# Kernel tuning notes

Hardware: AMD Instinct MI355X
Metric: run time of the kernel (lower is better)

## Reference

```python
import jax, jax.numpy as jnp
import numpy as np

D_MODEL = 2048
N_HEADS = 32
N_KVHEADS = 8
HEAD_DIM = D_MODEL // N_HEADS  # 64
N_GROUPS = N_HEADS // N_KVHEADS  # 4
B, L = 2, 2048


def setup_inputs() -> dict:
    key = jax.random.key(0)
    k1, k2, k3 = jax.random.split(key, 3)
    x = jax.random.normal(k1, (B, L, D_MODEL), dtype=jnp.float32)
    W_qkv = jax.random.normal(k2, (D_MODEL, HEAD_DIM * (N_HEADS + 2 * N_KVHEADS)), dtype=jnp.float32) * 0.02
    W_out = jax.random.normal(k3, (D_MODEL, D_MODEL), dtype=jnp.float32) * 0.02
    # additive causal mask, broadcasts over (b, g, h, l, j)
    neg = jnp.float32(-1e9)
    mask = jnp.where(jnp.tril(jnp.ones((L, L), dtype=bool)), jnp.float32(0.0), neg)
    return {"x": x, "mask": mask, "W_qkv": W_qkv, "W_out": W_out}


def reference(x, mask, W_qkv, W_out):
    b, l, _ = x.shape
    qkv = x @ W_qkv  # (b, l, hd*(H + 2*KVH))
    q, k, v = jnp.split(qkv, [N_HEADS * HEAD_DIM, (N_HEADS + N_KVHEADS) * HEAD_DIM], axis=-1)
    # NOTE: faithful to the original: plain row-major reshapes (no seq/head transpose)
    q = q.reshape(b, N_GROUPS, N_KVHEADS, l, HEAD_DIM)  # (b, g, h, l, d)
    k = k.reshape(b, N_KVHEADS, l, HEAD_DIM)            # (b, h, j, d)
    v = v.reshape(b, N_KVHEADS, l, HEAD_DIM)            # (b, h, j, d)
    scores = jnp.einsum('bghld,bhjd->bghlj', q, k) * (HEAD_DIM ** -0.5)
    scores = scores + mask  # mask broadcasts over leading dims
    attn = jax.nn.softmax(scores, axis=-1)
    out = jnp.einsum('bghlj,bhjd->bghld', attn, v)  # (b, g, h, l, d)
    # rearrange 'b g h l d -> b l (g h d)'
    out = jnp.transpose(out, (0, 3, 1, 2, 4)).reshape(b, l, D_MODEL)
    return out @ W_out
```

## Files before the change

kernel.cpp:

```cpp
#include <hip/hip_runtime.h>
#include <stdint.h>


typedef unsigned short u16;
typedef unsigned int u32;
typedef __attribute__((ext_vector_type(8))) short bf16x8;
typedef __attribute__((ext_vector_type(4))) float f32x4;

__device__ __forceinline__ u16 f2bf(float f) {
  union { float f; uint32_t u; } v; v.f = f;
  uint32_t u = v.u;
  u += 0x7fffu + ((u >> 16) & 1u);
  return (u16)(u >> 16);
}

__device__ __forceinline__ f32x4 mfma16(bf16x8 a, bf16x8 b, f32x4 c) {
  return __builtin_amdgcn_mfma_f32_16x16x32_bf16(a, b, c, 0, 0, 0);
}

__device__ __forceinline__ uint32_t cvt_pk_bf16(float a, float b) {
  uint32_t r;
  asm("v_cvt_pk_bf16_f32 %0, %1, %2" : "=v"(r) : "v"(a), "v"(b));
  return r;
}

__device__ __forceinline__ float fmax3(float a, float b, float c) {
  float d;
  asm("v_max3_f32 %0, %1, %2, %3" : "=v"(d) : "v"(a), "v"(b), "v"(c));
  return d;
}

__device__ __forceinline__ float exp2fast(float x) {
  return __builtin_amdgcn_exp2f(x);
}

__device__ __forceinline__ void gload16(const u16* g, u16* l) {
  __builtin_amdgcn_global_load_lds((__attribute__((address_space(1))) void*)g,
                                   (__attribute__((address_space(3))) void*)l, 16, 0, 0);
}

__global__ __launch_bounds__(256) void cvt_f32_bf16(const float* __restrict__ in,
                                                    u16* __restrict__ out, int n4) {
  int i = blockIdx.x * blockDim.x + threadIdx.x;
  if (i < n4) {
    float4 v = ((const float4*)in)[i];
    uint2 o;
    o.x = (uint32_t)f2bf(v.x) | ((uint32_t)f2bf(v.y) << 16);
    o.y = (uint32_t)f2bf(v.z) | ((uint32_t)f2bf(v.w) << 16);
    ((uint2*)out)[i] = o;
  }
}

__global__ __launch_bounds__(256) void transpose_cvt(const float* __restrict__ in,
                                                     u16* __restrict__ out, int R, int C) {
  __shared__ float tile[32][33];
  int c0 = blockIdx.x * 32, r0 = blockIdx.y * 32;
  int tx = threadIdx.x, ty = threadIdx.y;
#pragma unroll
  for (int k = 0; k < 32; k += 8)
    tile[ty + k][tx] = in[(size_t)(r0 + ty + k) * C + c0 + tx];
  __syncthreads();
#pragma unroll
  for (int k = 0; k < 32; k += 8)
    out[(size_t)(c0 + ty + k) * R + r0 + tx] = f2bf(tile[tx][ty + k]);
}

template <bool OUTF32>
__global__ __launch_bounds__(256) void gemm_bf16(const u16* __restrict__ A,
                                                 const u16* __restrict__ Bt,
                                                 void* __restrict__ C,
                                                 int M, int N, int K) {
  __shared__ __align__(16) u16 As[2][128 * 32];
  __shared__ __align__(16) u16 Bs[2][128 * 32];
  int tid = threadIdx.x;
  int lane = tid & 63, w = tid >> 6;
  int wm = (w >> 1) * 64, wn = (w & 1) * 64;

  int nwg = gridDim.x * gridDim.y;
  int lin = blockIdx.y * gridDim.x + blockIdx.x;
  int lin2 = (lin & 7) * (nwg >> 3) + (lin >> 3);
  int bxs = lin2 % gridDim.x, bys = lin2 / gridDim.x;
  int bm = bys * 128, bn = bxs * 128;

  int c = lane & 15, g = lane >> 4;

  const int srow = w * 16 + (lane >> 2);
  const int scol = (((lane & 3) ^ ((lane >> 3) & 3))) * 8;
  const u16* aP = A + (size_t)(bm + srow) * K + scol;
  const u16* bP = Bt + (size_t)(bn + srow) * K + scol;
  const size_t rowskip = (size_t)64 * K;

  f32x4 zero = {0.f, 0.f, 0.f, 0.f};
  f32x4 acc[4][4];
#pragma unroll
  for (int mi = 0; mi < 4; mi++)
#pragma unroll
    for (int ni = 0; ni < 4; ni++) acc[mi][ni] = zero;

  auto STAGE = [&](int kt, int buf) {
    u16* aL = &As[buf][(w * 16) * 32];
    u16* bL = &Bs[buf][(w * 16) * 32];
    gload16(aP + kt, aL);
    gload16(aP + kt + rowskip, aL + 64 * 32);
    gload16(bP + kt, bL);
    gload16(bP + kt + rowskip, bL + 64 * 32);
  };

  const int nk = K >> 5;
  STAGE(0, 0);
  __syncthreads();

  const int fq = (g ^ ((c >> 1) & 3)) * 8;

  for (int t = 0; t < nk; ++t) {
    const int cur = t & 1;
    if (t + 1 < nk) STAGE((t + 1) << 5, cur ^ 1);
    bf16x8 af[4], bfr[4];
#pragma unroll
    for (int i = 0; i < 4; i++) af[i] = *(const bf16x8*)&As[cur][(wm + i * 16 + c) * 32 + fq];
#pragma unroll
    for (int i = 0; i < 4; i++) bfr[i] = *(const bf16x8*)&Bs[cur][(wn + i * 16 + c) * 32 + fq];
#pragma unroll
    for (int mi = 0; mi < 4; mi++)
#pragma unroll
      for (int ni = 0; ni < 4; ni++)
        acc[mi][ni] = mfma16(af[mi], bfr[ni], acc[mi][ni]);
    __syncthreads();
  }

#pragma unroll
  for (int mi = 0; mi < 4; mi++)
#pragma unroll
    for (int ni = 0; ni < 4; ni++)
#pragma unroll
      for (int i = 0; i < 4; i++) {
        int row = bm + wm + mi * 16 + g * 4 + i;
        int col = bn + wn + ni * 16 + c;
        float v = acc[mi][ni][i];
        if (OUTF32)
          ((float*)C)[(size_t)row * N + col] = v;
        else
          ((u16*)C)[(size_t)row * N + col] = f2bf(v);
      }
}

__global__ __launch_bounds__(512, 4) void attn_fwd(const u16* __restrict__ qkv,
                                                   u16* __restrict__ attn) {
  __shared__ __align__(16) u16 Ks[2][64][72];
  __shared__ __align__(16) u16 Vs[2][64][72];
  __shared__ __align__(16) u16 Ps[8][2][16][64];
  const int tid = threadIdx.x;
  const int lane = tid & 63, w = tid >> 6;
  const int c = lane & 15, g = lane >> 4;
  const float C2 = 0.18033688011112042f;

  const int bid = blockIdx.x;
  const int slot = bid >> 3;
  const int head = (bid & 7) * 8 + (slot >> 3);
  const int p = slot & 7;
  const int qtA = p, qtB = 15 - p;
  const int b = head >> 5, gh = head & 31, h = gh & 7;
  const u16* qb = qkv + (size_t)b * 6291456;
  const int qbaseA = qtA * 128 + w * 16;
  const int qbaseB = qtB * 128 + w * 16;

  const u16* qpA = qb + (size_t)(gh * 64 + qtA * 4 + (w >> 1)) * 3072 + ((w & 1) * 16 + c) * 64;
  const u16* qpB = qb + (size_t)(gh * 64 + qtB * 4 + (w >> 1)) * 3072 + ((w & 1) * 16 + c) * 64;
  bf16x8 qfA[2], qfB[2];
#pragma unroll
  for (int kd = 0; kd < 2; kd++) {
    qfA[kd] = *(const bf16x8*)(qpA + kd * 32 + g * 8);
    qfB[kd] = *(const bf16x8*)(qpB + kd * 32 + g * 8);
  }

  const f32x4 zero = {0.f, 0.f, 0.f, 0.f};
  f32x4 oA[4], oB[4];
#pragma unroll
  for (int dt = 0; dt < 4; dt++) { oA[dt] = zero; oB[dt] = zero; }
  float mA = -1e30f, sA = 0.f, mB = -1e30f, sB = 0.f;

  const int kj = tid >> 3, kd8 = (tid & 7) * 8;
  const int ksw = (kj & 7) << 3;
  const int vj0 = (tid & 31) * 2, vd = (tid >> 5) * 4;
  uint4 kreg;
  uint2 va, vb;

  auto LOAD = [&](int t) {
    int j = t * 64 + kj;
    const u16* kr = qb + (size_t)(h * 256 + (j >> 3)) * 3072 + 2048 + (j & 7) * 64;
    kreg = *(const uint4*)(kr + kd8);
    int jv0 = t * 64 + vj0;
    const u16* vr0 = qb + (size_t)(h * 256 + (jv0 >> 3)) * 3072 + 2560 + (jv0 & 7) * 64;
    int jv1 = jv0 + 1;
    const u16* vr1 = qb + (size_t)(h * 256 + (jv1 >> 3)) * 3072 + 2560 + (jv1 & 7) * 64;
    va = *(const uint2*)(vr0 + vd);
    vb = *(const uint2*)(vr1 + vd);
  };
  auto EX = [](uint2 v, int e) -> uint32_t {
    uint32_t x = (e < 2) ? v.x : v.y;
    return (e & 1) ? (x >> 16) : (x & 0xffffu);
  };
  auto STORE = [&](int buf) {
    *(uint4*)&Ks[buf][kj][kd8 ^ ksw] = kreg;
#pragma unroll
    for (int e = 0; e < 4; e++) {
      uint32_t wv = EX(va, e) | (EX(vb, e) << 16);
      int d = vd + e;
      *(u32*)&Vs[buf][d][vj0 ^ ((d & 7) << 3)] = wv;
    }
  };

  auto scorePart = [&](int t, int qbase, bf16x8 (&qf)[2], bf16x8 (&kf)[4][2],
                       float& m_i, float& s_i, f32x4 (&o)[4], int part) {
    f32x4 sc[4];
    __builtin_amdgcn_s_setprio(1);
#pragma unroll
    for (int kvt = 0; kvt < 4; kvt++) {
      f32x4 s = mfma16(kf[kvt][0], qf[0], zero);
      sc[kvt] = mfma16(kf[kvt][1], qf[1], s);
    }
    __builtin_amdgcn_s_setprio(0);
    const int q = qbase + c;
    if (t * 64 + 63 > qbase) {
#pragma unroll
      for (int kvt = 0; kvt < 4; kvt++)
#pragma unroll
        for (int i = 0; i < 4; i++)
          if (t * 64 + kvt * 16 + g * 4 + i > q) sc[kvt][i] = -1e30f;
    }
    float tmax = fmax3(sc[0][0], sc[0][1], sc[0][2]);
    tmax = fmax3(tmax, sc[0][3], sc[1][0]);
    tmax = fmax3(tmax, sc[1][1], sc[1][2]);
    tmax = fmax3(tmax, sc[1][3], sc[2][0]);
    tmax = fmax3(tmax, sc[2][1], sc[2][2]);
    tmax = fmax3(tmax, sc[2][3], sc[3][0]);
    tmax = fmax3(tmax, sc[3][1], sc[3][2]);
    tmax = fmaxf(tmax, sc[3][3]);
    tmax = fmaxf(tmax, __shfl_xor(tmax, 16));
    tmax = fmaxf(tmax, __shfl_xor(tmax, 32));
    if (!__all(tmax <= m_i + 64.0f)) {
      float mn = fmaxf(m_i, tmax);
      float corr = exp2fast((m_i - mn) * C2);
      m_i = mn;
      s_i *= corr;
#pragma unroll
      for (int i = 0; i < 4; i++) {
        float cb = __shfl(corr, g * 4 + i);
#pragma unroll
        for (int dt = 0; dt < 4; dt++) o[dt][i] *= cb;
      }
    }
    const float nmc = -m_i * C2;
    float rs = 0.f;
#pragma unroll
    for (int kvt = 0; kvt < 4; kvt++)
#pragma unroll
      for (int i = 0; i < 4; i++) {
        float pv = exp2fast(fmaf(sc[kvt][i], C2, nmc));
        sc[kvt][i] = pv;
        rs += pv;
      }
    rs += __shfl_xor(rs, 16);
    rs += __shfl_xor(rs, 32);
    s_i += rs;
    const int sw = (c & 7) << 3;
#pragma unroll
    for (int kvt = 0; kvt < 4; kvt++) {
      uint2 pw;
      pw.x = cvt_pk_bf16(sc[kvt][0], sc[kvt][1]);
      pw.y = cvt_pk_bf16(sc[kvt][2], sc[kvt][3]);
      *(uint2*)&Ps[w][part][c][(kvt * 16 + g * 4) ^ sw] = pw;
    }
  };

  const int nt = 2 * qtB + 2;
  const int jtA = (qbaseA + 15) >> 6;
  const int jtB = (qbaseB + 15) >> 6;

  LOAD(0);
  STORE(0);
  __syncthreads();

  for (int t = 0; t < nt; ++t) {
    const int cur = t & 1;
    if (t + 1 < nt) LOAD(t + 1);
    if (t <= jtB) {
      const int sw = (c & 7) << 3;
      bf16x8 kf[4][2];
#pragma unroll
      for (int kvt = 0; kvt < 4; kvt++)
#pragma unroll
        for (int kd = 0; kd < 2; kd++)
          kf[kvt][kd] = *(const bf16x8*)&Ks[cur][kvt * 16 + c][(kd * 32 + g * 8) ^ sw];
      const bool doA = (t <= jtA);
      if (doA) scorePart(t, qbaseA, qfA, kf, mA, sA, oA, 0);
      scorePart(t, qbaseB, qfB, kf, mB, sB, oB, 1);
      __builtin_amdgcn_s_setprio(1);
#pragma unroll
      for (int kt2 = 0; kt2 < 2; kt2++) {
        bf16x8 bv[4];
#pragma unroll
        for (int dt = 0; dt < 4; dt++)
          bv[dt] = *(const bf16x8*)&Vs[cur][dt * 16 + c][(kt2 * 32 + g * 8) ^ sw];
        if (doA) {
          bf16x8 pa = *(const bf16x8*)&Ps[w][0][c][(kt2 * 32 + g * 8) ^ sw];
#pragma unroll
          for (int dt = 0; dt < 4; dt++) oA[dt] = mfma16(pa, bv[dt], oA[dt]);
        }
        {
          bf16x8 pb = *(const bf16x8*)&Ps[w][1][c][(kt2 * 32 + g * 8) ^ sw];
#pragma unroll
          for (int dt = 0; dt < 4; dt++) oB[dt] = mfma16(pb, bv[dt], oB[dt]);
        }
      }
      __builtin_amdgcn_s_setprio(0);
    }
    if (t + 1 < nt) STORE(cur ^ 1);
    __syncthreads();
  }

  auto epi = [&](int qbase, f32x4 (&o)[4], float s_i) {
#pragma unroll
    for (int i = 0; i < 4; i++) {
      float sd = __shfl(s_i, g * 4 + i);
      float inv = 1.0f / sd;
      int row = qbase + g * 4 + i;
      u16* orow = attn + ((size_t)(b * 2048 + row)) * 2048 + gh * 64;
#pragma unroll
      for (int dt = 0; dt < 4; dt++) orow[dt * 16 + c] = f2bf(o[dt][i] * inv);
    }
  };
  epi(qbaseA, oA, sA);
  epi(qbaseB, oB, sB);
}

extern "C" void kernel_launch(void* const* d_in, const int* in_sizes, int n_in,
                              void* d_out, int out_size, void* d_ws, size_t ws_size,
                              hipStream_t stream) {
  const float* x = (const float*)d_in[0];
  const float* Wqkv = (const float*)d_in[2];
  const float* Wout = (const float*)d_in[3];
  float* out = (float*)d_out;

  u16* xb = (u16*)d_ws;
  u16* wqkvT = xb + 8388608;
  u16* woutT = wqkvT + 6291456;
  u16* qkv = woutT + 4194304;
  u16* attn = qkv + 12582912;

  cvt_f32_bf16<<<8192, 256, 0, stream>>>(x, xb, 2097152);
  transpose_cvt<<<dim3(3072 / 32, 2048 / 32), dim3(32, 8), 0, stream>>>(Wqkv, wqkvT, 2048, 3072);
  transpose_cvt<<<dim3(2048 / 32, 2048 / 32), dim3(32, 8), 0, stream>>>(Wout, woutT, 2048, 2048);
  gemm_bf16<false><<<dim3(3072 / 128, 4096 / 128), 256, 0, stream>>>(xb, wqkvT, qkv, 4096, 3072, 2048);
  attn_fwd<<<512, 512, 0, stream>>>(qkv, attn);
  gemm_bf16<true><<<dim3(2048 / 128, 4096 / 128), 256, 0, stream>>>(attn, woutT, out, 4096, 2048, 2048);
}
```

Measured before the change: 218.3 us.

## Halve attention query tile to 64 rows with 256-thread blocks and 1024-block grid

The attention kernel now processes paired 64-row query tiles (p and 31-p) per block with 4 waves instead of 128-row tiles with 8 waves. The grid doubles to 1024 blocks and launch bounds become 256 threads with 3 blocks per CU, aiming for finer-grained load balancing and more resident blocks. K/V staging is rewritten so each thread loads wider K chunks and four V rows, with the K swizzle dropped and a new V swizzle. The trade-off is that each K/V tile is reused by fewer queries, which increases K/V global/L2 traffic per block, and dropping the K swizzle may reintroduce LDS bank conflicts.

Result: slower. 224.9 us (+3.0%).

```diff
diff --git a/kernel.cpp b/kernel.cpp
--- a/kernel.cpp
+++ b/kernel.cpp
@@ -144,11 +144,11 @@
       }
 }
 
-__global__ __launch_bounds__(512, 4) void attn_fwd(const u16* __restrict__ qkv,
+__global__ __launch_bounds__(256, 3) void attn_fwd(const u16* __restrict__ qkv,
                                                    u16* __restrict__ attn) {
   __shared__ __align__(16) u16 Ks[2][64][72];
   __shared__ __align__(16) u16 Vs[2][64][72];
-  __shared__ __align__(16) u16 Ps[8][2][16][64];
+  __shared__ __align__(16) u16 Ps[4][2][16][64];
   const int tid = threadIdx.x;
   const int lane = tid & 63, w = tid >> 6;
   const int c = lane & 15, g = lane >> 4;
@@ -156,16 +156,16 @@
 
   const int bid = blockIdx.x;
   const int slot = bid >> 3;
-  const int head = (bid & 7) * 8 + (slot >> 3);
-  const int p = slot & 7;
-  const int qtA = p, qtB = 15 - p;
+  const int head = (bid & 7) * 8 + (slot >> 4);
+  const int p = slot & 15;
+  const int qtA = p, qtB = 31 - p;
   const int b = head >> 5, gh = head & 31, h = gh & 7;
   const u16* qb = qkv + (size_t)b * 6291456;
-  const int qbaseA = qtA * 128 + w * 16;
-  const int qbaseB = qtB * 128 + w * 16;
-
-  const u16* qpA = qb + (size_t)(gh * 64 + qtA * 4 + (w >> 1)) * 3072 + ((w & 1) * 16 + c) * 64;
-  const u16* qpB = qb + (size_t)(gh * 64 + qtB * 4 + (w >> 1)) * 3072 + ((w & 1) * 16 + c) * 64;
+  const int qbaseA = qtA * 64 + w * 16;
+  const int qbaseB = qtB * 64 + w * 16;
+
+  const u16* qpA = qb + (size_t)(gh * 64 + qtA * 2 + (w >> 1)) * 3072 + ((w & 1) * 16 + c) * 64;
+  const u16* qpB = qb + (size_t)(gh * 64 + qtB * 2 + (w >> 1)) * 3072 + ((w & 1) * 16 + c) * 64;
   bf16x8 qfA[2], qfB[2];
 #pragma unroll
   for (int kd = 0; kd < 2; kd++) {
@@ -179,34 +179,37 @@
   for (int dt = 0; dt < 4; dt++) { oA[dt] = zero; oB[dt] = zero; }
   float mA = -1e30f, sA = 0.f, mB = -1e30f, sB = 0.f;
 
-  const int kj = tid >> 3, kd8 = (tid & 7) * 8;
-  const int ksw = (kj & 7) << 3;
-  const int vj0 = (tid & 31) * 2, vd = (tid >> 5) * 4;
-  uint4 kreg;
-  uint2 va, vb;
+  const int kj = tid >> 2, kd16 = (tid & 3) * 16;
+  const int vj0 = (tid >> 4) * 4, vd = (tid & 15) * 4;
+  const int vsw = (tid & 7) << 3;
+  uint4 kreg0, kreg1;
+  uint2 vreg[4];
 
   auto LOAD = [&](int t) {
     int j = t * 64 + kj;
     const u16* kr = qb + (size_t)(h * 256 + (j >> 3)) * 3072 + 2048 + (j & 7) * 64;
-    kreg = *(const uint4*)(kr + kd8);
-    int jv0 = t * 64 + vj0;
-    const u16* vr0 = qb + (size_t)(h * 256 + (jv0 >> 3)) * 3072 + 2560 + (jv0 & 7) * 64;
-    int jv1 = jv0 + 1;
-    const u16* vr1 = qb + (size_t)(h * 256 + (jv1 >> 3)) * 3072 + 2560 + (jv1 & 7) * 64;
-    va = *(const uint2*)(vr0 + vd);
-    vb = *(const uint2*)(vr1 + vd);
+    kreg0 = *(const uint4*)(kr + kd16);
+    kreg1 = *(const uint4*)(kr + kd16 + 8);
+#pragma unroll
+    for (int r = 0; r < 4; r++) {
+      int jv = t * 64 + vj0 + r;
+      const u16* vr = qb + (size_t)(h * 256 + (jv >> 3)) * 3072 + 2560 + (jv & 7) * 64;
+      vreg[r] = *(const uint2*)(vr + vd);
+    }
   };
   auto EX = [](uint2 v, int e) -> uint32_t {
     uint32_t x = (e < 2) ? v.x : v.y;
     return (e & 1) ? (x >> 16) : (x & 0xffffu);
   };
   auto STORE = [&](int buf) {
-    *(uint4*)&Ks[buf][kj][kd8 ^ ksw] = kreg;
+    *(uint4*)&Ks[buf][kj][kd16] = kreg0;
+    *(uint4*)&Ks[buf][kj][kd16 + 8] = kreg1;
 #pragma unroll
     for (int e = 0; e < 4; e++) {
-      uint32_t wv = EX(va, e) | (EX(vb, e) << 16);
-      int d = vd + e;
-      *(u32*)&Vs[buf][d][vj0 ^ ((d & 7) << 3)] = wv;
+      uint2 wv;
+      wv.x = EX(vreg[0], e) | (EX(vreg[1], e) << 16);
+      wv.y = EX(vreg[2], e) | (EX(vreg[3], e) << 16);
+      *(uint2*)&Vs[buf][vd + e][vj0 ^ vsw] = wv;
     }
   };
 
@@ -273,9 +276,8 @@
     }
   };
 
-  const int nt = 2 * qtB + 2;
-  const int jtA = (qbaseA + 15) >> 6;
-  const int jtB = (qbaseB + 15) >> 6;
+  const int nt = qtB + 1;
+  const int jtA = qtA;
 
   LOAD(0);
   STORE(0);
@@ -284,24 +286,27 @@
   for (int t = 0; t < nt; ++t) {
     const int cur = t & 1;
     if (t + 1 < nt) LOAD(t + 1);
-    if (t <= jtB) {
-      const int sw = (c & 7) << 3;
+    {
       bf16x8 kf[4][2];
 #pragma unroll
       for (int kvt = 0; kvt < 4; kvt++)
 #pragma unroll
         for (int kd = 0; kd < 2; kd++)
-          kf[kvt][kd] = *(const bf16x8*)&Ks[cur][kvt * 16 + c][(kd * 32 + g * 8) ^ sw];
+          kf[kvt][kd] = *(const bf16x8*)&Ks[cur][kvt * 16 + c][kd * 32 + g * 8];
       const bool doA = (t <= jtA);
       if (doA) scorePart(t, qbaseA, qfA, kf, mA, sA, oA, 0);
       scorePart(t, qbaseB, qfB, kf, mB, sB, oB, 1);
+      const int sw = (c & 7) << 3;
       __builtin_amdgcn_s_setprio(1);
 #pragma unroll
       for (int kt2 = 0; kt2 < 2; kt2++) {
         bf16x8 bv[4];
 #pragma unroll
-        for (int dt = 0; dt < 4; dt++)
-          bv[dt] = *(const bf16x8*)&Vs[cur][dt * 16 + c][(kt2 * 32 + g * 8) ^ sw];
+        for (int dt = 0; dt < 4; dt++) {
+          const int vr = dt * 16 + c;
+          const int sv = ((dt * 4 + (c >> 2)) & 7) << 3;
+          bv[dt] = *(const bf16x8*)&Vs[cur][vr][(kt2 * 32 + g * 8) ^ sv];
+        }
         if (doA) {
           bf16x8 pa = *(const bf16x8*)&Ps[w][0][c][(kt2 * 32 + g * 8) ^ sw];
 #pragma unroll
@@ -352,6 +357,6 @@
   transpose_cvt<<<dim3(3072 / 32, 2048 / 32), dim3(32, 8), 0, stream>>>(Wqkv, wqkvT, 2048, 3072);
   transpose_cvt<<<dim3(2048 / 32, 2048 / 32), dim3(32, 8), 0, stream>>>(Wout, woutT, 2048, 2048);
   gemm_bf16<false><<<dim3(3072 / 128, 4096 / 128), 256, 0, stream>>>(xb, wqkvT, qkv, 4096, 3072, 2048);
-  attn_fwd<<<512, 512, 0, stream>>>(qkv, attn);
+  attn_fwd<<<1024, 256, 0, stream>>>(qkv, attn);
   gemm_bf16<true><<<dim3(2048 / 128, 4096 / 128), 256, 0, stream>>>(attn, woutT, out, 4096, 2048, 2048);
 }
```
